# Kernel tuning notes

Hardware: AMD Instinct MI355X
Metric: run time of the kernel (lower is better)

Reference implementation:

```python
import jax, jax.numpy as jnp
import numpy as np

THRESHOLD = 0.9  # module buffer _threshold (starting_threshold)


def setup_inputs() -> dict:
    key = jax.random.key(0)
    k_x, k_w = jax.random.split(key)
    B, T, D = 64, 577, 768
    x = jax.random.normal(k_x, (B, T, D), dtype=jnp.float32)
    # nn.Linear(in_dim, 1): weight [1, D] -> stored as vector [D], bias [1]
    w = jax.random.normal(k_w, (D,), dtype=jnp.float32) * (1.0 / np.sqrt(D))
    b = jnp.zeros((1,), dtype=jnp.float32)
    return {"x": x, "w": w, "b": b}


def reference(x, w, b):
    B, T, D = x.shape
    density = int(T * THRESHOLD)  # static: int(577*0.9) = 519
    # head: Linear(D,1) -> sigmoid -> [B, T]  (dropout is identity in eval)
    prob = jax.nn.sigmoid(jnp.einsum('btd,d->bt', x, w) + b[0])
    # keep top-`density` tokens by score (sorted descending, like torch.topk)
    _, top_idx = jax.lax.top_k(prob, density)
    tokens = jnp.take_along_axis(x, top_idx[..., None], axis=1)  # [B, density, D]
    # bottom (T - density) tokens: topk(largest=False) == topk of -prob,
    # which yields values sorted ascending in prob, matching torch
    n_skip = T - density  # 58 > 0
    neg_vals, skip_idx = jax.lax.top_k(-prob, n_skip)
    skip_tokens = jnp.take_along_axis(x, skip_idx[..., None], axis=1)  # [B, n_skip, D]
    weights = jax.nn.softmax(-neg_vals, axis=-1)  # softmax over skipped probs
    summary_token = jnp.sum(skip_tokens * weights[..., None], axis=1, keepdims=True)  # [B,1,D]
    return tokens, skip_tokens, summary_token
```

## Files before the change

### kernel.cpp

```cpp
#include <hip/hip_runtime.h>
#include <math.h>

#define BB 64
#define TT 577
#define DD 768
#define DENS 519
#define NSKIP 58
#define NROWS (BB * TT)

typedef float vf4 __attribute__((ext_vector_type(4)));

__device__ inline unsigned long long key_of(double z) {
    long long b = __double_as_longlong(z);
    return (b < 0) ? ~(unsigned long long)b
                   : ((unsigned long long)b | 0x8000000000000000ULL);
}
__device__ inline double key_inv(unsigned long long k) {
    long long b = (k >> 63) ? (long long)(k & 0x7fffffffffffffffULL)
                            : ~(long long)k;
    return __longlong_as_double(b);
}

__global__ __launch_bounds__(256) void k_prob(const float* __restrict__ x,
                                              const float* __restrict__ w,
                                              const float* __restrict__ bias,
                                              unsigned long long* __restrict__ keys) {
    int wave = (int)((blockIdx.x * blockDim.x + threadIdx.x) >> 6);
    int lane = threadIdx.x & 63;
    if (wave >= NROWS) return;
    const float4* r4 = (const float4*)(x + (size_t)wave * DD);
    const float4* w4 = (const float4*)w;
    double acc = 0.0;
#pragma unroll
    for (int i = 0; i < 3; ++i) {
        float4 a = r4[lane + 64 * i];
        float4 b = w4[lane + 64 * i];
        acc += (double)a.x * (double)b.x + (double)a.y * (double)b.y
             + (double)a.z * (double)b.z + (double)a.w * (double)b.w;
    }
#pragma unroll
    for (int off = 32; off; off >>= 1)
        acc += __shfl_down(acc, off, 64);
    if (lane == 0) {
        keys[wave] = key_of(acc + (double)bias[0]);
    }
}

__global__ __launch_bounds__(256) void k_rankscatter(const float* __restrict__ x,
                                                     const unsigned long long* __restrict__ keys,
                                                     int* __restrict__ skip_src,
                                                     unsigned long long* __restrict__ skip_key,
                                                     float* __restrict__ out) {
    int wave = (int)((blockIdx.x * blockDim.x + threadIdx.x) >> 6);
    int lane = threadIdx.x & 63;
    if (wave >= NROWS) return;
    int b = wave / TT;
    int i = wave - b * TT;
    const unsigned long long* kb = keys + b * TT;
    unsigned long long ki = kb[i];
    int rd = 0, ra = 0;
#pragma unroll
    for (int c = 0; c < 10; ++c) {
        int j = lane + 64 * c;
        if (j < TT) {
            unsigned long long kj = kb[j];
            bool tie = (kj == ki) & (j < i);
            rd += ((kj > ki) | tie) ? 1 : 0;
            ra += ((kj < ki) | tie) ? 1 : 0;
        }
    }
    unsigned long long pack = ((unsigned long long)(unsigned)rd << 32) | (unsigned)ra;
#pragma unroll
    for (int off = 32; off; off >>= 1)
        pack += __shfl_xor(pack, off, 64);
    int r_desc = (int)(pack >> 32);
    int r_asc  = (int)(pack & 0xffffffffu);

    size_t dst;
    if (r_desc < DENS) {
        dst = (size_t)(b * DENS + r_desc) * DD;
    } else {
        dst = (size_t)BB * DENS * DD + (size_t)(b * NSKIP + r_asc) * DD;
        if (lane == 0) {
            skip_src[b * NSKIP + r_asc] = i;
            skip_key[b * NSKIP + r_asc] = ki;
        }
    }
    const vf4* s4 = (const vf4*)(x + ((size_t)b * TT + i) * DD);
    vf4* d4 = (vf4*)(out + dst);
#pragma unroll
    for (int c = 0; c < 3; ++c) {
        vf4 v = s4[lane + 64 * c];
        __builtin_nontemporal_store(v, &d4[lane + 64 * c]);
    }
}

__global__ __launch_bounds__(768) void k_soft(const float* __restrict__ x,
                                              const int* __restrict__ skip_src,
                                              const unsigned long long* __restrict__ skip_key,
                                              float* __restrict__ summary) {
    __shared__ float wsh[NSKIP];
    __shared__ int   ssh[NSKIP];
    int b = blockIdx.x;
    int t = threadIdx.x;
    if (t < NSKIP) ssh[t] = skip_src[b * NSKIP + t];
    if (t < 64) {
        double pv = -1.0e300;
        if (t < NSKIP) {
            double z = key_inv(skip_key[b * NSKIP + t]);
            pv = 1.0 / (1.0 + exp(-z));
        }
        double m = pv;
#pragma unroll
        for (int off = 32; off; off >>= 1) {
            double o = __shfl_down(m, off, 64);
            m = (o > m) ? o : m;
        }
        m = __shfl(m, 0, 64);
        double e = (t < NSKIP) ? exp(pv - m) : 0.0;
        double s = e;
#pragma unroll
        for (int off = 32; off; off >>= 1)
            s += __shfl_down(s, off, 64);
        s = __shfl(s, 0, 64);
        if (t < NSKIP) wsh[t] = (float)(e / s);
    }
    __syncthreads();
    float acc = 0.f;
    const float* xb = x + (size_t)b * TT * DD;
    for (int k = 0; k < NSKIP; ++k)
        acc += wsh[k] * xb[(size_t)ssh[k] * DD + t];
    summary[(size_t)b * DD + t] = acc;
}

extern "C" void kernel_launch(void* const* d_in, const int* in_sizes, int n_in,
                              void* d_out, int out_size, void* d_ws, size_t ws_size,
                              hipStream_t stream) {
    const float* x    = (const float*)d_in[0];
    const float* w    = (const float*)d_in[1];
    const float* bias = (const float*)d_in[2];
    float* out = (float*)d_out;
    char* ws = (char*)d_ws;

    unsigned long long* keys = (unsigned long long*)ws;
    int* skip_src = (int*)(ws + 295424);
    unsigned long long* skip_key =
        (unsigned long long*)(ws + 295424 + 14848);

    const int nblk = NROWS / 4;

    k_prob<<<nblk, 256, 0, stream>>>(x, w, bias, keys);
    k_rankscatter<<<nblk, 256, 0, stream>>>(x, keys, skip_src, skip_key, out);
    k_soft<<<BB, 768, 0, stream>>>(x, skip_src, skip_key,
                                   out + (size_t)BB * (DENS + NSKIP) * DD);
}
```

Before: 225.2 us.

## Fuse three kernels into one cooperative persistent kernel with grid syncs

Replaces the three separate launches (score, rank+scatter, softmax summary) with a single cooperative kernel of 1024 blocks that grid-strides over rows and uses grid.sync between phases. The weight vector is kept in registers across rows, and the summary phase is split over 4 blocks per batch instead of one 768-thread block. This targets launch gaps and per-launch tail effects. It adds grid-wide barrier cost and depends on the cooperative launch succeeding, falling back to the old three kernels if it does not.

```diff
diff --git a/kernel.cpp b/kernel.cpp
--- a/kernel.cpp
+++ b/kernel.cpp
@@ -1,5 +1,8 @@
 #include <hip/hip_runtime.h>
+#include <hip/hip_cooperative_groups.h>
 #include <math.h>
+
+namespace cg = cooperative_groups;
 
 #define BB 64
 #define TT 577
@@ -8,6 +11,10 @@
 #define NSKIP 58
 #define NROWS (BB * TT)
 
+#define GRID 1024
+#define BLK 256
+#define NWAVES (GRID * (BLK / 64))
+
 typedef float vf4 __attribute__((ext_vector_type(4)));
 
 __device__ inline unsigned long long key_of(double z) {
@@ -19,6 +26,126 @@
     long long b = (k >> 63) ? (long long)(k & 0x7fffffffffffffffULL)
                             : ~(long long)k;
     return __longlong_as_double(b);
+}
+
+__global__ __launch_bounds__(BLK, 4) void k_fused(
+        const float* __restrict__ x, const float* __restrict__ w,
+        const float* __restrict__ bias,
+        unsigned long long* __restrict__ keys,
+        int* __restrict__ skip_src,
+        unsigned long long* __restrict__ skip_key,
+        float* __restrict__ out) {
+    cg::grid_group grid = cg::this_grid();
+    const int wave = (int)((blockIdx.x * BLK + threadIdx.x) >> 6);
+    const int lane = threadIdx.x & 63;
+
+    {
+        const float4* w4 = (const float4*)w;
+        const float4 wv0 = w4[lane];
+        const float4 wv1 = w4[lane + 64];
+        const float4 wv2 = w4[lane + 128];
+        const double bz = (double)bias[0];
+        for (int r = wave; r < NROWS; r += NWAVES) {
+            const float4* r4 = (const float4*)(x + (size_t)r * DD);
+            float4 a0 = r4[lane];
+            float4 a1 = r4[lane + 64];
+            float4 a2 = r4[lane + 128];
+            double acc = (double)a0.x * (double)wv0.x + (double)a0.y * (double)wv0.y
+                       + (double)a0.z * (double)wv0.z + (double)a0.w * (double)wv0.w;
+            acc += (double)a1.x * (double)wv1.x + (double)a1.y * (double)wv1.y
+                 + (double)a1.z * (double)wv1.z + (double)a1.w * (double)wv1.w;
+            acc += (double)a2.x * (double)wv2.x + (double)a2.y * (double)wv2.y
+                 + (double)a2.z * (double)wv2.z + (double)a2.w * (double)wv2.w;
+#pragma unroll
+            for (int off = 32; off; off >>= 1)
+                acc += __shfl_down(acc, off, 64);
+            if (lane == 0) keys[r] = key_of(acc + bz);
+        }
+    }
+    grid.sync();
+
+    for (int r = wave; r < NROWS; r += NWAVES) {
+        int b = r / TT;
+        int i = r - b * TT;
+        const unsigned long long* kb = keys + b * TT;
+        unsigned long long ki = kb[i];
+        int rd = 0, ra = 0;
+#pragma unroll
+        for (int c = 0; c < 10; ++c) {
+            int j = lane + 64 * c;
+            if (j < TT) {
+                unsigned long long kj = kb[j];
+                bool tie = (kj == ki) & (j < i);
+                rd += ((kj > ki) | tie) ? 1 : 0;
+                ra += ((kj < ki) | tie) ? 1 : 0;
+            }
+        }
+        unsigned long long pack = ((unsigned long long)(unsigned)rd << 32) | (unsigned)ra;
+#pragma unroll
+        for (int off = 32; off; off >>= 1)
+            pack += __shfl_xor(pack, off, 64);
+        int r_desc = (int)(pack >> 32);
+        int r_asc  = (int)(pack & 0xffffffffu);
+
+        size_t dst;
+        if (r_desc < DENS) {
+            dst = (size_t)(b * DENS + r_desc) * DD;
+        } else {
+            dst = (size_t)BB * DENS * DD + (size_t)(b * NSKIP + r_asc) * DD;
+            if (lane == 0) {
+                skip_src[b * NSKIP + r_asc] = i;
+                skip_key[b * NSKIP + r_asc] = ki;
+            }
+        }
+        const vf4* s4 = (const vf4*)(x + (size_t)r * DD);
+        vf4* d4 = (vf4*)(out + dst);
+#pragma unroll
+        for (int c = 0; c < 3; ++c) {
+            vf4 v = s4[lane + 64 * c];
+            __builtin_nontemporal_store(v, &d4[lane + 64 * c]);
+        }
+    }
+    grid.sync();
+
+    __shared__ float wsh[NSKIP];
+    __shared__ int   ssh[NSKIP];
+    int blk = blockIdx.x;
+    if (blk < 4 * BB) {
+        int b = blk >> 2, q = blk & 3;
+        int t = threadIdx.x;
+        if (t < NSKIP) ssh[t] = skip_src[b * NSKIP + t];
+        if (t < 64) {
+            double pv = -1.0e300;
+            if (t < NSKIP) {
+                double z = key_inv(skip_key[b * NSKIP + t]);
+                pv = 1.0 / (1.0 + exp(-z));
+            }
+            double m = pv;
+#pragma unroll
+            for (int off = 32; off; off >>= 1) {
+                double o = __shfl_down(m, off, 64);
+                m = (o > m) ? o : m;
+            }
+            m = __shfl(m, 0, 64);
+            double e = (t < NSKIP) ? exp(pv - m) : 0.0;
+            double s = e;
+#pragma unroll
+            for (int off = 32; off; off >>= 1)
+                s += __shfl_down(s, off, 64);
+            s = __shfl(s, 0, 64);
+            if (t < NSKIP) wsh[t] = (float)(e / s);
+        }
+        __syncthreads();
+        if (t < 192) {
+            int d = q * 192 + t;
+            const float* xb = x + (size_t)b * TT * DD;
+            float acc = 0.f;
+#pragma unroll
+            for (int k = 0; k < NSKIP; ++k)
+                acc += wsh[k] * xb[(size_t)ssh[k] * DD + d];
+            out[(size_t)BB * TT * DD + (size_t)b * DD + d] = acc;
+        }
+    }
 }
 
 __global__ __launch_bounds__(256) void k_prob(const float* __restrict__ x,
@@ -41,9 +168,7 @@
 #pragma unroll
     for (int off = 32; off; off >>= 1)
         acc += __shfl_down(acc, off, 64);
-    if (lane == 0) {
-        keys[wave] = key_of(acc + (double)bias[0]);
-    }
+    if (lane == 0) keys[wave] = key_of(acc + (double)bias[0]);
 }
 
 __global__ __launch_bounds__(256) void k_rankscatter(const float* __restrict__ x,
@@ -75,7 +200,6 @@
         pack += __shfl_xor(pack, off, 64);
     int r_desc = (int)(pack >> 32);
     int r_asc  = (int)(pack & 0xffffffffu);
-
     size_t dst;
     if (r_desc < DENS) {
         dst = (size_t)(b * DENS + r_desc) * DD;
@@ -147,10 +271,16 @@
     unsigned long long* skip_key =
         (unsigned long long*)(ws + 295424 + 14848);
 
-    const int nblk = NROWS / 4;
-
-    k_prob<<<nblk, 256, 0, stream>>>(x, w, bias, keys);
-    k_rankscatter<<<nblk, 256, 0, stream>>>(x, keys, skip_src, skip_key, out);
-    k_soft<<<BB, 768, 0, stream>>>(x, skip_src, skip_key,
-                                   out + (size_t)BB * (DENS + NSKIP) * DD);
-}
+    void* args[] = { (void*)&x, (void*)&w, (void*)&bias, (void*)&keys,
+                     (void*)&skip_src, (void*)&skip_key, (void*)&out };
+    hipError_t err = hipLaunchCooperativeKernel((const void*)k_fused,
+                                                dim3(GRID), dim3(BLK),
+                                                args, 0u, stream);
+    if (err != hipSuccess) {
+        const int nblk = NROWS / 4;
+        k_prob<<<nblk, 256, 0, stream>>>(x, w, bias, keys);
+        k_rankscatter<<<nblk, 256, 0, stream>>>(x, keys, skip_src, skip_key, out);
+        k_soft<<<BB, 768, 0, stream>>>(x, skip_src, skip_key,
+                                       out + (size_t)BB * (DENS + NSKIP) * DD);
+    }
+}
```

Measured after the change: 428.6 us. 90.3% more time.

## Fuse score, rank and summary into per-batch kernel; separate row scatter copy

Applied to the files above, without the earlier changes.

Score computation, ranking, softmax weighting and the summary reduction are merged into one kernel with one 1024-thread block per batch. Keys and skip indices stay in shared memory, and ranks come from a per-thread serial scan over LDS instead of a wave-parallel scan of global keys. A second kernel then copies each row to its destination using a precomputed destination-row table. This removes the global key and skip buffers and one launch, but the fused kernel runs only 64 blocks, so most CUs sit idle while it reads all of x.

```diff
diff --git a/kernel.cpp b/kernel.cpp
--- a/kernel.cpp
+++ b/kernel.cpp
@@ -21,93 +21,69 @@
     return __longlong_as_double(b);
 }
 
-__global__ __launch_bounds__(256) void k_prob(const float* __restrict__ x,
-                                              const float* __restrict__ w,
-                                              const float* __restrict__ bias,
-                                              unsigned long long* __restrict__ keys) {
-    int wave = (int)((blockIdx.x * blockDim.x + threadIdx.x) >> 6);
-    int lane = threadIdx.x & 63;
-    if (wave >= NROWS) return;
-    const float4* r4 = (const float4*)(x + (size_t)wave * DD);
-    const float4* w4 = (const float4*)w;
-    double acc = 0.0;
+__global__ __launch_bounds__(1024) void k_rank(const float* __restrict__ x,
+                                               const float* __restrict__ w,
+                                               const float* __restrict__ bias,
+                                               int* __restrict__ dstRow,
+                                               float* __restrict__ out) {
+    __shared__ unsigned long long key[TT];
+    __shared__ int   skipIdx[NSKIP];
+    __shared__ float wsh[NSKIP];
+    const int b    = blockIdx.x;
+    const int tid  = threadIdx.x;
+    const int wid  = tid >> 6;
+    const int lane = tid & 63;
+    const float* xb = x + (size_t)b * TT * DD;
+
+    {
+        const float4* w4 = (const float4*)w;
+        const float4 wv0 = w4[lane];
+        const float4 wv1 = w4[lane + 64];
+        const float4 wv2 = w4[lane + 128];
+        const double bz = (double)bias[0];
+        for (int t = wid; t < TT; t += 16) {
+            const float4* r4 = (const float4*)(xb + (size_t)t * DD);
+            float4 a0 = r4[lane];
+            float4 a1 = r4[lane + 64];
+            float4 a2 = r4[lane + 128];
+            double acc = (double)a0.x * (double)wv0.x + (double)a0.y * (double)wv0.y
+                       + (double)a0.z * (double)wv0.z + (double)a0.w * (double)wv0.w;
+            acc += (double)a1.x * (double)wv1.x + (double)a1.y * (double)wv1.y
+                 + (double)a1.z * (double)wv1.z + (double)a1.w * (double)wv1.w;
+            acc += (double)a2.x * (double)wv2.x + (double)a2.y * (double)wv2.y
+                 + (double)a2.z * (double)wv2.z + (double)a2.w * (double)wv2.w;
 #pragma unroll
-    for (int i = 0; i < 3; ++i) {
-        float4 a = r4[lane + 64 * i];
-        float4 b = w4[lane + 64 * i];
-        acc += (double)a.x * (double)b.x + (double)a.y * (double)b.y
-             + (double)a.z * (double)b.z + (double)a.w * (double)b.w;
-    }
-#pragma unroll
-    for (int off = 32; off; off >>= 1)
-        acc += __shfl_down(acc, off, 64);
-    if (lane == 0) {
-        keys[wave] = key_of(acc + (double)bias[0]);
-    }
-}
-
-__global__ __launch_bounds__(256) void k_rankscatter(const float* __restrict__ x,
-                                                     const unsigned long long* __restrict__ keys,
-                                                     int* __restrict__ skip_src,
-                                                     unsigned long long* __restrict__ skip_key,
-                                                     float* __restrict__ out) {
-    int wave = (int)((blockIdx.x * blockDim.x + threadIdx.x) >> 6);
-    int lane = threadIdx.x & 63;
-    if (wave >= NROWS) return;
-    int b = wave / TT;
-    int i = wave - b * TT;
-    const unsigned long long* kb = keys + b * TT;
-    unsigned long long ki = kb[i];
-    int rd = 0, ra = 0;
-#pragma unroll
-    for (int c = 0; c < 10; ++c) {
-        int j = lane + 64 * c;
-        if (j < TT) {
-            unsigned long long kj = kb[j];
-            bool tie = (kj == ki) & (j < i);
-            rd += ((kj > ki) | tie) ? 1 : 0;
-            ra += ((kj < ki) | tie) ? 1 : 0;
+            for (int off = 32; off; off >>= 1)
+                acc += __shfl_down(acc, off, 64);
+            if (lane == 0) key[t] = key_of(acc + bz);
         }
     }
-    unsigned long long pack = ((unsigned long long)(unsigned)rd << 32) | (unsigned)ra;
-#pragma unroll
-    for (int off = 32; off; off >>= 1)
-        pack += __shfl_xor(pack, off, 64);
-    int r_desc = (int)(pack >> 32);
-    int r_asc  = (int)(pack & 0xffffffffu);
+    __syncthreads();
 
-    size_t dst;
-    if (r_desc < DENS) {
-        dst = (size_t)(b * DENS + r_desc) * DD;
-    } else {
-        dst = (size_t)BB * DENS * DD + (size_t)(b * NSKIP + r_asc) * DD;
-        if (lane == 0) {
-            skip_src[b * NSKIP + r_asc] = i;
-            skip_key[b * NSKIP + r_asc] = ki;
+    if (tid < TT) {
+        const unsigned long long ki = key[tid];
+        int rd = 0;
+#pragma unroll 8
+        for (int j = 0; j < TT; ++j) {
+            unsigned long long kj = key[j];
+            rd += ((kj > ki) | ((kj == ki) & (j < tid))) ? 1 : 0;
         }
+        int dst;
+        if (rd < DENS) {
+            dst = b * DENS + rd;
+        } else {
+            int ra = (TT - 1) - rd;
+            dst = BB * DENS + b * NSKIP + ra;
+            skipIdx[ra] = tid;
+        }
+        dstRow[b * TT + tid] = dst;
     }
-    const vf4* s4 = (const vf4*)(x + ((size_t)b * TT + i) * DD);
-    vf4* d4 = (vf4*)(out + dst);
-#pragma unroll
-    for (int c = 0; c < 3; ++c) {
-        vf4 v = s4[lane + 64 * c];
-        __builtin_nontemporal_store(v, &d4[lane + 64 * c]);
-    }
-}
+    __syncthreads();
 
-__global__ __launch_bounds__(768) void k_soft(const float* __restrict__ x,
-                                              const int* __restrict__ skip_src,
-                                              const unsigned long long* __restrict__ skip_key,
-                                              float* __restrict__ summary) {
-    __shared__ float wsh[NSKIP];
-    __shared__ int   ssh[NSKIP];
-    int b = blockIdx.x;
-    int t = threadIdx.x;
-    if (t < NSKIP) ssh[t] = skip_src[b * NSKIP + t];
-    if (t < 64) {
+    if (tid < 64) {
         double pv = -1.0e300;
-        if (t < NSKIP) {
-            double z = key_inv(skip_key[b * NSKIP + t]);
+        if (tid < NSKIP) {
+            double z = key_inv(key[skipIdx[tid]]);
             pv = 1.0 / (1.0 + exp(-z));
         }
         double m = pv;
@@ -117,20 +93,39 @@
             m = (o > m) ? o : m;
         }
         m = __shfl(m, 0, 64);
-        double e = (t < NSKIP) ? exp(pv - m) : 0.0;
+        double e = (tid < NSKIP) ? exp(pv - m) : 0.0;
         double s = e;
 #pragma unroll
         for (int off = 32; off; off >>= 1)
             s += __shfl_down(s, off, 64);
         s = __shfl(s, 0, 64);
-        if (t < NSKIP) wsh[t] = (float)(e / s);
+        if (tid < NSKIP) wsh[tid] = (float)(e / s);
     }
     __syncthreads();
-    float acc = 0.f;
-    const float* xb = x + (size_t)b * TT * DD;
-    for (int k = 0; k < NSKIP; ++k)
-        acc += wsh[k] * xb[(size_t)ssh[k] * DD + t];
-    summary[(size_t)b * DD + t] = acc;
+
+    if (tid < DD) {
+        float acc = 0.f;
+#pragma unroll
+        for (int k = 0; k < NSKIP; ++k)
+            acc += wsh[k] * xb[(size_t)skipIdx[k] * DD + tid];
+        out[(size_t)NROWS * DD + (size_t)b * DD + tid] = acc;
+    }
+}
+
+__global__ __launch_bounds__(256) void k_copy(const float* __restrict__ x,
+                                              const int* __restrict__ dstRow,
+                                              float* __restrict__ out) {
+    int wave = (int)((blockIdx.x * blockDim.x + threadIdx.x) >> 6);
+    int lane = threadIdx.x & 63;
+    if (wave >= NROWS) return;
+    int dst = dstRow[wave];
+    const vf4* s4 = (const vf4*)(x + (size_t)wave * DD);
+    vf4* d4 = (vf4*)(out + (size_t)dst * DD);
+#pragma unroll
+    for (int c = 0; c < 3; ++c) {
+        vf4 v = s4[lane + 64 * c];
+        __builtin_nontemporal_store(v, &d4[lane + 64 * c]);
+    }
 }
 
 extern "C" void kernel_launch(void* const* d_in, const int* in_sizes, int n_in,
@@ -140,17 +135,8 @@
     const float* w    = (const float*)d_in[1];
     const float* bias = (const float*)d_in[2];
     float* out = (float*)d_out;
-    char* ws = (char*)d_ws;
+    int* dstRow = (int*)d_ws;
 
-    unsigned long long* keys = (unsigned long long*)ws;
-    int* skip_src = (int*)(ws + 295424);
-    unsigned long long* skip_key =
-        (unsigned long long*)(ws + 295424 + 14848);
-
-    const int nblk = NROWS / 4;
-
-    k_prob<<<nblk, 256, 0, stream>>>(x, w, bias, keys);
-    k_rankscatter<<<nblk, 256, 0, stream>>>(x, keys, skip_src, skip_key, out);
-    k_soft<<<BB, 768, 0, stream>>>(x, skip_src, skip_key,
-                                   out + (size_t)BB * (DENS + NSKIP) * DD);
+    k_rank<<<BB, 1024, 0, stream>>>(x, w, bias, dstRow, out);
+    k_copy<<<NROWS / 4, 256, 0, stream>>>(x, dstRow, out);
 }
```

Result: slower. 247.9 us (+10.1%).
